# Optimization experiments

Hardware: AMD Instinct MI355X
Metric: run time of the kernel (lower is better)

Reference implementation:

```python
import jax, jax.numpy as jnp
import numpy as np

N_EMBD = 1024
N_HEAD = 16
HORIZON = 64
HS = N_EMBD // N_HEAD        # 64
BD = max(HS // 4, 16)        # 16


def setup_inputs() -> dict:
    key = jax.random.key(0)
    ks = jax.random.split(key, 12)
    s = 0.02
    B, T = 2, 1024
    return {
        "x": jax.random.normal(ks[0], (B, T, N_EMBD), jnp.float32),
        "W_disp": jax.random.normal(ks[1], (N_EMBD, N_HEAD * BD), jnp.float32) * s,
        "W_val": jax.random.normal(ks[2], (N_EMBD, N_EMBD), jnp.float32) * s,
        "rel_pos_emb": jax.random.normal(ks[3], (HORIZON, BD), jnp.float32) * s,
        "W_strain": jax.random.normal(ks[4], (BD, BD), jnp.float32) * s,
        "W_pos": jax.random.normal(ks[5], (BD, BD), jnp.float32) * s,
        "W_bond": jax.random.normal(ks[6], (BD, 1), jnp.float32) * s,
        "W_dmg": jax.random.normal(ks[7], (BD, BD), jnp.float32) * s,
        "b_dmg": jnp.zeros((BD,), jnp.float32),
        "W_dmg_out": jax.random.normal(ks[8], (BD, 1), jnp.float32) * s,
        "b_dmg_out": jnp.full((1,), -3.0, jnp.float32),  # nn.init.constant_(damage_out.bias, -3.0)
        "W_cproj": jax.random.normal(ks[9], (N_EMBD, N_EMBD), jnp.float32) * s,
    }


def _windows(t, delta):
    # t: (B, nh, T, D) -> (B, nh, T, delta, D); causal sliding window via left pad
    B, nh, T, D = t.shape
    padded = jnp.pad(t, ((0, 0), (0, 0), (delta - 1, 0), (0, 0)))
    idx = jnp.arange(T)[:, None] + jnp.arange(delta)[None, :]  # (T, delta)
    return padded[:, :, idx]  # gather over time axis


def reference(x, W_disp, W_val, rel_pos_emb, W_strain, W_pos, W_bond,
              W_dmg, b_dmg, W_dmg_out, b_dmg_out, W_cproj):
    B, T, C = x.shape
    nh, bd, hs = N_HEAD, BD, HS
    delta = min(HORIZON, T)

    disp = (x @ W_disp).reshape(B, T, nh, bd).transpose(0, 2, 1, 3)  # (B,nh,T,bd)
    val = (x @ W_val).reshape(B, T, nh, hs).transpose(0, 2, 1, 3)    # (B,nh,T,hs)

    disp_win = _windows(disp, delta)  # (B,nh,T,delta,bd)
    val_win = _windows(val, delta)    # (B,nh,T,delta,hs)

    # causal mask: window slot w for token t maps to position t - delta + 1 + w
    cmask = (jnp.arange(T)[:, None] - delta + 1 + jnp.arange(delta)[None, :]) >= 0  # (T,delta)

    strain = disp_win - disp[:, :, :, None, :]  # (B,nh,T,delta,bd)
    rel_emb = rel_pos_emb[:delta]               # (delta,bd)

    bond_act = jax.nn.gelu(strain @ W_strain + rel_emb @ W_pos, approximate=False)
    bond_logits = (bond_act @ W_bond)[..., 0]   # (B,nh,T,delta)

    damage_act = jax.nn.gelu(strain @ W_dmg + b_dmg, approximate=False)
    damage = jax.nn.sigmoid((damage_act @ W_dmg_out)[..., 0] + b_dmg_out[0])

    logits = bond_logits - 10.0 * damage
    logits = jnp.where(cmask[None, None], logits, -jnp.inf)
    weights = jax.nn.softmax(logits, axis=-1)

    out = jnp.einsum('bntd,bntde->bnte', weights, val_win)  # (B,nh,T,hs)
    out = out.transpose(0, 2, 1, 3).reshape(B, T, C)
    return out @ W_cproj
```

## Files before the change

kernel.cpp:

```cpp
#include <hip/hip_runtime.h>
#include <hip/hip_bf16.h>
#include <hip/hip_fp16.h>
#include <math.h>

#define TB   2
#define TT   1024
#define TC   1024
#define NH   16
#define HS   64
#define BDI  16
#define DLT  64
#define LDD  1280
#define GK   1024

typedef __attribute__((ext_vector_type(8))) short short8;
typedef __attribute__((ext_vector_type(4))) float floatx4;
typedef __attribute__((ext_vector_type(16))) float floatx16;
typedef __hip_bfloat16 bf16;

__device__ __forceinline__ unsigned pkbf(float a, float b) {
    return (__float_as_uint(a) >> 16) | (__float_as_uint(b) & 0xFFFF0000u);
}

__device__ __forceinline__ unsigned bfbits(float x) {
    bf16 h = __float2bfloat16(x);
    return (unsigned)*(unsigned short*)&h;
}

__device__ __forceinline__ __half2 gelu_pk(__half2 x, __half2 kc1, __half2 kc2,
                                           __half2 khalf) {
    __half2 y = __hmul2(x, x);
    __half2 p = __hfma2(y, kc2, kc1);
    return __hfma2(x, khalf, __hmul2(y, p));
}

__device__ __forceinline__ void gload_lds16(const void* g, void* l) {
    __builtin_amdgcn_global_load_lds(
        (const __attribute__((address_space(1))) unsigned int*)(unsigned long long)g,
        (__attribute__((address_space(3))) unsigned int*)(unsigned int)(unsigned long long)l,
        16, 0, 0);
}

__device__ __forceinline__ void tpose_body(const float* __restrict__ in,
                                           bf16* __restrict__ outp,
                                           int k0, int n0, int N,
                                           float (*tile)[33], int tid) {
    const int tx = tid & 31, ty4 = (tid >> 5) * 4;
#pragma unroll
    for (int i = 0; i < 4; i++)
        tile[ty4 + i][tx] = in[(long long)(k0 + ty4 + i) * N + n0 + tx];
    __syncthreads();
#pragma unroll
    for (int i = 0; i < 4; i++)
        outp[(long long)(n0 + ty4 + i) * TC + k0 + tx] = __float2bfloat16(tile[tx][ty4 + i]);
}

__global__ __launch_bounds__(256) void prep_k(
    const float* __restrict__ x, const float* __restrict__ Wdisp,
    const float* __restrict__ Wval, const float* __restrict__ Wc,
    bf16* __restrict__ xb, bf16* __restrict__ Wdvt, bf16* __restrict__ Wct) {
    __shared__ float tile[32][33];
    const int blk = blockIdx.x, tid = threadIdx.x;
    if (blk < 2048) {
        int i = blk * 1024 + tid * 4;
        float4 v = *(const float4*)(x + i);
        bf16 o0 = __float2bfloat16(v.x), o1 = __float2bfloat16(v.y);
        bf16 o2 = __float2bfloat16(v.z), o3 = __float2bfloat16(v.w);
        ushort4 u;
        u.x = *(unsigned short*)&o0; u.y = *(unsigned short*)&o1;
        u.z = *(unsigned short*)&o2; u.w = *(unsigned short*)&o3;
        *(ushort4*)(xb + i) = u;
    } else if (blk < 2304) {
        int l = blk - 2048;
        tpose_body(Wdisp, Wdvt, (l >> 3) * 32, (l & 7) * 32, 256, tile, tid);
    } else if (blk < 3328) {
        int l = blk - 2304;
        tpose_body(Wval, Wdvt + (size_t)256 * TC, (l >> 5) * 32, (l & 31) * 32, TC, tile, tid);
    } else {
        int l = blk - 3328;
        tpose_body(Wc, Wct, (l >> 5) * 32, (l & 31) * 32, TC, tile, tid);
    }
}

template <int ID>
__global__ __launch_bounds__(256) void mfma_gemm_k(const bf16* __restrict__ A,
                                                   const bf16* __restrict__ Bt,
                                                   float* __restrict__ C,
                                                   int M, int N, int nbx) {
    __shared__ __align__(16) bf16 As[2][64 * 128];
    __shared__ __align__(16) bf16 Bs[2][64 * 128];
    const int tid = threadIdx.x;
    const int w = tid >> 6, lane = tid & 63;

    const int xcd = blockIdx.x & 7, s0 = blockIdx.x >> 3;
    const int l = xcd * (gridDim.x >> 3) + s0;
    const int row0 = (l / nbx) * 64, col0 = (l % nbx) * 64;
    const int wm = (w >> 1) * 32, wn = (w & 1) * 32;

    const bf16* gA[4];
    const bf16* gB[4];
    int lofs[4];
#pragma unroll
    for (int p = 0; p < 4; p++) {
        int u = (p * 4 + w) * 64 + lane;
        int r = u >> 4, s = u & 15;
        int c = s ^ (r & 15);
        gA[p] = A  + (long long)(row0 + r) * GK + c * 8;
        gB[p] = Bt + (long long)(col0 + r) * GK + c * 8;
        lofs[p] = (p * 4 + w) * 512;
    }

    floatx4 acc[2][2] = {};
    const int rA = lane & 15, quad = lane >> 4;

#pragma unroll
    for (int p = 0; p < 4; p++) {
        gload_lds16(gA[p], &As[0][lofs[p]]);
        gload_lds16(gB[p], &Bs[0][lofs[p]]);
    }

    int cur = 0;
    for (int k0 = 0; k0 < GK; k0 += 128) {
        __syncthreads();
        if (k0 + 128 < GK) {
#pragma unroll
            for (int p = 0; p < 4; p++) {
                gload_lds16(gA[p] + k0 + 128, &As[cur ^ 1][lofs[p]]);
                gload_lds16(gB[p] + k0 + 128, &Bs[cur ^ 1][lofs[p]]);
            }
        }
        const bf16* Ac = As[cur];
        const bf16* Bc = Bs[cur];
#pragma unroll
        for (int kh = 0; kh < 4; kh++) {
            const int g = kh * 4 + quad;
            short8 af[2], bfr[2];
#pragma unroll
            for (int i = 0; i < 2; i++) {
                af[i]  = *(const short8*)&Ac[(wm + i * 16 + rA) * 128 + ((g ^ rA) * 8)];
                bfr[i] = *(const short8*)&Bc[(wn + i * 16 + rA) * 128 + ((g ^ rA) * 8)];
            }
#pragma unroll
            for (int i = 0; i < 2; i++)
#pragma unroll
                for (int j = 0; j < 2; j++)
                    acc[i][j] = __builtin_amdgcn_mfma_f32_16x16x32_bf16(af[i], bfr[j], acc[i][j], 0, 0, 0);
        }
        cur ^= 1;
    }
    const int cn = lane & 15, rq = (lane >> 4) * 4;
#pragma unroll
    for (int i = 0; i < 2; i++)
#pragma unroll
        for (int j = 0; j < 2; j++) {
            long long base = (long long)(row0 + wm + i * 16 + rq) * N + col0 + wn + j * 16 + cn;
#pragma unroll
            for (int r = 0; r < 4; r++)
                C[base + (long long)r * N] = acc[i][j][r];
        }
}

__global__ __launch_bounds__(256) void attn_k(
    const float* __restrict__ dv,
    const float* __restrict__ rel,
    const float* __restrict__ W_strain,
    const float* __restrict__ W_dmg,
    const float* __restrict__ Wp,
    const float* __restrict__ W_bond,
    const float* __restrict__ b_dmg,
    const float* __restrict__ W_dmg_out,
    const float* __restrict__ b_dmg_out,
    bf16* __restrict__ attnout) {
    __shared__ __align__(16) float          sDisp[79][20];
    __shared__ __align__(16) unsigned short sValT[64][104];
    __shared__ __align__(16) unsigned short sWgtS[16][104];

    const int tid = threadIdx.x;
    const int wave = tid >> 6, lane = tid & 63;
    const int xcd = blockIdx.x & 7, slot = blockIdx.x >> 3;
    const int bh = xcd * 4 + (slot >> 6);
    const int t0 = (slot & 63) * 16;
    const int h = bh & (NH - 1);
    const int b = bh >> 4;

    if (tid < 208) ((int4*)sWgtS)[tid] = make_int4(0, 0, 0, 0);

    for (int idx = tid; idx < 79 * 4; idx += 256) {
        int r = idx >> 2, c = idx & 3;
        int row = t0 - 63 + r; row = row < 0 ? 0 : row;
        *(float4*)&sDisp[r][c * 4] =
            *(const float4*)(dv + (long long)(b * TT + row) * LDD + h * BDI + c * 4);
    }
    for (int idx = tid; idx < 24 * 16; idx += 256) {
        int k4 = (idx >> 4) * 4, e4 = (idx & 15) * 4;
        float vv[4][4];
#pragma unroll
        for (int rr = 0; rr < 4; rr++) {
            int row = t0 - 63 + k4 + rr;
            row = row < 0 ? 0 : (row > TT - 1 ? TT - 1 : row);
            *(float4*)vv[rr] =
                *(const float4*)(dv + (long long)(b * TT + row) * LDD + 256 + h * HS + e4);
        }
#pragma unroll
        for (int e = 0; e < 4; e++) {
            uint2 wv;
            wv.x = bfbits(vv[0][e]) | (bfbits(vv[1][e]) << 16);
            wv.y = bfbits(vv[2][e]) | (bfbits(vv[3][e]) << 16);
            *(uint2*)&sValT[e4 + e][k4] = wv;
        }
    }

    const int n = lane & 31, hi = lane >> 5;
    union U8 { short8 s8; unsigned u[4]; };
    const floatx16 z16 = {};

    short8 aw, ape;
    {
        const float* wsel = (n < 16) ? (W_strain + n) : (W_dmg + (n - 16));
        float wv[8], pv[8];
#pragma unroll
        for (int e = 0; e < 8; e++) {
            wv[e] = wsel[(8 * hi + e) * BDI];
            pv[e] = (n < 16) ? Wp[(8 * hi + e) * BDI + n] : 0.f;
        }
        U8 a, p;
#pragma unroll
        for (int q = 0; q < 4; q++) {
            a.u[q] = pkbf(wv[2 * q], wv[2 * q + 1]);
            p.u[q] = pkbf(pv[2 * q], pv[2 * q + 1]);
        }
        aw = a.s8; ape = p.s8;
    }
    floatx16 cb[2];
#pragma unroll
    for (int h2 = 0; h2 < 2; h2++) {
        float rv[8];
        const float* rp = rel + (32 * h2 + n) * BDI + 8 * hi;
        *(float4*)&rv[0] = *(const float4*)rp;
        *(float4*)&rv[4] = *(const float4*)(rp + 4);
        U8 r_;
#pragma unroll
        for (int q = 0; q < 4; q++) r_.u[q] = pkbf(rv[2 * q], rv[2 * q + 1]);
        cb[h2] = __builtin_amdgcn_mfma_f32_32x32x16_bf16(ape, r_.s8, z16, 0, 0, 0);
    }
    {
        float4 bdA = *(const float4*)(b_dmg + 4 * hi);
        float4 bdB = *(const float4*)(b_dmg + 8 + 4 * hi);
#pragma unroll
        for (int h2 = 0; h2 < 2; h2++) {
            cb[h2][8]  += bdA.x; cb[h2][9]  += bdA.y;
            cb[h2][10] += bdA.z; cb[h2][11] += bdA.w;
            cb[h2][12] += bdB.x; cb[h2][13] += bdB.y;
            cb[h2][14] += bdB.z; cb[h2][15] += bdB.w;
        }
    }
    __half2 wbp[4], wdp[4];
    {
        float4 wbA = *(const float4*)(W_bond + 4 * hi);
        float4 wbB = *(const float4*)(W_bond + 8 + 4 * hi);
        float4 wdA = *(const float4*)(W_dmg_out + 4 * hi);
        float4 wdB = *(const float4*)(W_dmg_out + 8 + 4 * hi);
        wbp[0] = __floats2half2_rn(wbA.x, wbA.y); wbp[1] = __floats2half2_rn(wbA.z, wbA.w);
        wbp[2] = __floats2half2_rn(wbB.x, wbB.y); wbp[3] = __floats2half2_rn(wbB.z, wbB.w);
        wdp[0] = __floats2half2_rn(wdA.x, wdA.y); wdp[1] = __floats2half2_rn(wdA.z, wdA.w);
        wdp[2] = __floats2half2_rn(wdB.x, wdB.y); wdp[3] = __floats2half2_rn(wdB.z, wdB.w);
    }
    const float bdo0 = b_dmg_out[0];
    const __half2 kc1   = __floats2half2_rn(0.3989422804f, 0.3989422804f);
    const __half2 kc2   = __floats2half2_rn(-0.06649038006f, -0.06649038006f);
    const __half2 khalf = __floats2half2_rn(0.5f, 0.5f);

    __syncthreads();

#pragma unroll
    for (int s = 0; s < 4; s++) {
        const int tau = 4 * wave + s;
        float oc[8];
        {
            const float* op = &sDisp[tau + 63][8 * hi];
            *(float4*)&oc[0] = *(const float4*)op;
            *(float4*)&oc[4] = *(const float4*)(op + 4);
        }
        floatx16 c2r[2];
#pragma unroll
        for (int h2 = 0; h2 < 2; h2++) {
            const float* rp = &sDisp[tau + 32 * h2 + n][8 * hi];
            float p[8];
            *(float4*)&p[0] = *(const float4*)rp;
            *(float4*)&p[4] = *(const float4*)(rp + 4);
            U8 t_;
#pragma unroll
            for (int pp = 0; pp < 4; pp++)
                t_.u[pp] = pkbf(p[2 * pp] - oc[2 * pp], p[2 * pp + 1] - oc[2 * pp + 1]);
            c2r[h2] = __builtin_amdgcn_mfma_f32_32x32x16_bf16(aw, t_.s8, cb[h2], 0, 0, 0);
        }
        float ee[2];
#pragma unroll
        for (int h2 = 0; h2 < 2; h2++) {
            __half2 accb = __floats2half2_rn(0.f, 0.f);
            __half2 accd = __floats2half2_rn(0.f, 0.f);
#pragma unroll
            for (int i = 0; i < 4; i++) {
                __half2 xb_ = __floats2half2_rn(c2r[h2][2 * i], c2r[h2][2 * i + 1]);
                __half2 xd_ = __floats2half2_rn(c2r[h2][8 + 2 * i], c2r[h2][9 + 2 * i]);
                accb = __hfma2(gelu_pk(xb_, kc1, kc2, khalf), wbp[i], accb);
                accd = __hfma2(gelu_pk(xd_, kc1, kc2, khalf), wdp[i], accd);
            }
            float bond = __low2float(accb) + __high2float(accb);
            float dmgv = __low2float(accd) + __high2float(accd);
            bond += __shfl_xor(bond, 32);
            dmgv += __shfl_xor(dmgv, 32);
            float damage = 1.f / (1.f + __expf(-(dmgv + bdo0)));
            const int j = 32 * h2 + n;
            const bool valid = (t0 + tau + j - 63) >= 0;
            ee[h2] = valid ? __expf(bond - 10.f * damage) : 0.f;
        }
        float sm = ee[0] + ee[1];
#pragma unroll
        for (int off = 16; off >= 1; off >>= 1) sm += __shfl_xor(sm, off);
        float inv = 1.0f / sm;
        if (hi == 0) {
            sWgtS[tau][tau + n]      = (unsigned short)bfbits(ee[0] * inv);
            sWgtS[tau][tau + 32 + n] = (unsigned short)bfbits(ee[1] * inv);
        }
    }
    __syncthreads();

    const int m = lane & 15, quad = lane >> 4;
    const floatx4 zf = {0.f, 0.f, 0.f, 0.f};
    floatx4 acc = zf;
#pragma unroll
    for (int c = 0; c < 3; c++) {
        short8 afr = *(const short8*)&sWgtS[m][c * 32 + quad * 8];
        short8 bfr = *(const short8*)&sValT[16 * wave + m][c * 32 + quad * 8];
        acc = __builtin_amdgcn_mfma_f32_16x16x32_bf16(afr, bfr, acc, 0, 0, 0);
    }
    const int e0 = 16 * wave + m;
#pragma unroll
    for (int r = 0; r < 4; r++) {
        int tau = quad * 4 + r;
        attnout[(long long)(b * TT + t0 + tau) * TC + h * HS + e0] = __float2bfloat16(acc[r]);
    }
}

extern "C" void kernel_launch(void* const* d_in, const int* in_sizes, int n_in,
                              void* d_out, int out_size, void* d_ws, size_t ws_size,
                              hipStream_t stream) {
    const float* x      = (const float*)d_in[0];
    const float* W_disp = (const float*)d_in[1];
    const float* W_val  = (const float*)d_in[2];
    const float* rel    = (const float*)d_in[3];
    const float* Ws     = (const float*)d_in[4];
    const float* Wp     = (const float*)d_in[5];
    const float* Wb     = (const float*)d_in[6];
    const float* Wd     = (const float*)d_in[7];
    const float* bd_    = (const float*)d_in[8];
    const float* Wdo    = (const float*)d_in[9];
    const float* bdo    = (const float*)d_in[10];
    const float* Wc     = (const float*)d_in[11];
    float* out = (float*)d_out;

    const int M = TB * TT;
    char* ws = (char*)d_ws;
    bf16*  xb    = (bf16*)ws;
    bf16*  attnb = (bf16*)ws;
    bf16*  Wdvt  = (bf16*)(ws + (size_t)4 * 1024 * 1024);
    bf16*  Wct   = (bf16*)(ws + (size_t)6656 * 1024);
    float* dvC   = (float*)(ws + (size_t)8704 * 1024);

    dim3 blk(256);
    prep_k<<<4352, blk, 0, stream>>>(x, W_disp, W_val, Wc, xb, Wdvt, Wct);
    mfma_gemm_k<1><<<(M / 64) * (LDD / 64), blk, 0, stream>>>(xb, Wdvt, dvC, M, LDD, LDD / 64);
    attn_k<<<(TB * NH * TT) / 16, blk, 0, stream>>>(dvC, rel, Ws, Wd, Wp, Wb, bd_,
                                                    Wdo, bdo, attnb);
    mfma_gemm_k<2><<<(M / 64) * (TC / 64), blk, 0, stream>>>(attnb, Wct, out, M, TC, TC / 64);
}
```

Before: 135.8 us.

## Emit transposed bf16 values from QKV GEMM epilogue and precompute positional bias

The first GEMM now writes the value projection directly as per-head transposed bf16 (head, e, t). The attention kernel can then read MFMA B fragments straight from global memory instead of staging and converting them through shared memory. The rel_pos_emb @ W_pos product is precomputed once in the prep kernel and added in fp16 rather than computed per block with an MFMA. The change also adds an occupancy hint (launch_bounds 256,8) and shifts the weight-column indexing by one slot. In exchange it adds uncoalesced short global writes in the GEMM epilogue and unstaged global reads of values in attention.

Measured after the change: 131.8 us. 2.9% less time.

```diff
diff --git a/kernel.cpp b/kernel.cpp
--- a/kernel.cpp
+++ b/kernel.cpp
@@ -10,8 +10,8 @@
 #define HS   64
 #define BDI  16
 #define DLT  64
-#define LDD  1280
 #define GK   1024
+#define NDV  1280
 
 typedef __attribute__((ext_vector_type(8))) short short8;
 typedef __attribute__((ext_vector_type(4))) float floatx4;
@@ -58,7 +58,9 @@
 __global__ __launch_bounds__(256) void prep_k(
     const float* __restrict__ x, const float* __restrict__ Wdisp,
     const float* __restrict__ Wval, const float* __restrict__ Wc,
-    bf16* __restrict__ xb, bf16* __restrict__ Wdvt, bf16* __restrict__ Wct) {
+    const float* __restrict__ rel, const float* __restrict__ Wp,
+    bf16* __restrict__ xb, bf16* __restrict__ Wdvt, bf16* __restrict__ Wct,
+    float* __restrict__ peG) {
     __shared__ float tile[32][33];
     const int blk = blockIdx.x, tid = threadIdx.x;
     if (blk < 2048) {
@@ -76,9 +78,17 @@
     } else if (blk < 3328) {
         int l = blk - 2304;
         tpose_body(Wval, Wdvt + (size_t)256 * TC, (l >> 5) * 32, (l & 31) * 32, TC, tile, tid);
-    } else {
+    } else if (blk < 4352) {
         int l = blk - 3328;
         tpose_body(Wc, Wct, (l >> 5) * 32, (l & 31) * 32, TC, tile, tid);
+    } else {
+        int idx = (blk - 4352) * 256 + tid;
+        int j = idx >> 4, d = idx & 15;
+        float s = 0.f;
+#pragma unroll
+        for (int k = 0; k < BDI; k++)
+            s += rel[j * BDI + k] * Wp[k * BDI + d];
+        peG[idx] = s;
     }
 }
 
@@ -86,6 +96,7 @@
 __global__ __launch_bounds__(256) void mfma_gemm_k(const bf16* __restrict__ A,
                                                    const bf16* __restrict__ Bt,
                                                    float* __restrict__ C,
+                                                   bf16* __restrict__ valT,
                                                    int M, int N, int nbx) {
     __shared__ __align__(16) bf16 As[2][64 * 128];
     __shared__ __align__(16) bf16 Bs[2][64 * 128];
@@ -149,30 +160,45 @@
         cur ^= 1;
     }
     const int cn = lane & 15, rq = (lane >> 4) * 4;
-#pragma unroll
-    for (int i = 0; i < 2; i++)
-#pragma unroll
-        for (int j = 0; j < 2; j++) {
-            long long base = (long long)(row0 + wm + i * 16 + rq) * N + col0 + wn + j * 16 + cn;
-#pragma unroll
-            for (int r = 0; r < 4; r++)
-                C[base + (long long)r * N] = acc[i][j][r];
-        }
-}
-
-__global__ __launch_bounds__(256) void attn_k(
-    const float* __restrict__ dv,
-    const float* __restrict__ rel,
+    if (ID == 1 && col0 >= 256) {
+        const int hh = (col0 - 256) >> 6;
+        const int bb = row0 >> 10;
+#pragma unroll
+        for (int i = 0; i < 2; i++)
+#pragma unroll
+            for (int j = 0; j < 2; j++) {
+                int e = wn + j * 16 + cn;
+                int trow = row0 - bb * TT + wm + i * 16 + rq;
+                uint2 st;
+                st.x = bfbits(acc[i][j][0]) | (bfbits(acc[i][j][1]) << 16);
+                st.y = bfbits(acc[i][j][2]) | (bfbits(acc[i][j][3]) << 16);
+                *(uint2*)(valT + ((size_t)((bb * NH + hh) * HS + e) * TT + trow)) = st;
+            }
+    } else {
+#pragma unroll
+        for (int i = 0; i < 2; i++)
+#pragma unroll
+            for (int j = 0; j < 2; j++) {
+                long long base = (long long)(row0 + wm + i * 16 + rq) * N + col0 + wn + j * 16 + cn;
+#pragma unroll
+                for (int r = 0; r < 4; r++)
+                    C[base + (long long)r * N] = acc[i][j][r];
+            }
+    }
+}
+
+__global__ __launch_bounds__(256, 8) void attn_k(
+    const float* __restrict__ dispC,
+    const bf16* __restrict__ valT,
+    const float* __restrict__ peG,
     const float* __restrict__ W_strain,
     const float* __restrict__ W_dmg,
-    const float* __restrict__ Wp,
     const float* __restrict__ W_bond,
     const float* __restrict__ b_dmg,
     const float* __restrict__ W_dmg_out,
     const float* __restrict__ b_dmg_out,
     bf16* __restrict__ attnout) {
     __shared__ __align__(16) float          sDisp[79][20];
-    __shared__ __align__(16) unsigned short sValT[64][104];
     __shared__ __align__(16) unsigned short sWgtS[16][104];
 
     const int tid = threadIdx.x;
@@ -189,73 +215,38 @@
         int r = idx >> 2, c = idx & 3;
         int row = t0 - 63 + r; row = row < 0 ? 0 : row;
         *(float4*)&sDisp[r][c * 4] =
-            *(const float4*)(dv + (long long)(b * TT + row) * LDD + h * BDI + c * 4);
-    }
-    for (int idx = tid; idx < 24 * 16; idx += 256) {
-        int k4 = (idx >> 4) * 4, e4 = (idx & 15) * 4;
-        float vv[4][4];
-#pragma unroll
-        for (int rr = 0; rr < 4; rr++) {
-            int row = t0 - 63 + k4 + rr;
-            row = row < 0 ? 0 : (row > TT - 1 ? TT - 1 : row);
-            *(float4*)vv[rr] =
-                *(const float4*)(dv + (long long)(b * TT + row) * LDD + 256 + h * HS + e4);
-        }
-#pragma unroll
-        for (int e = 0; e < 4; e++) {
-            uint2 wv;
-            wv.x = bfbits(vv[0][e]) | (bfbits(vv[1][e]) << 16);
-            wv.y = bfbits(vv[2][e]) | (bfbits(vv[3][e]) << 16);
-            *(uint2*)&sValT[e4 + e][k4] = wv;
-        }
+            *(const float4*)(dispC + (long long)(b * TT + row) * 256 + h * BDI + c * 4);
     }
 
     const int n = lane & 31, hi = lane >> 5;
     union U8 { short8 s8; unsigned u[4]; };
     const floatx16 z16 = {};
 
-    short8 aw, ape;
+    short8 aw;
     {
         const float* wsel = (n < 16) ? (W_strain + n) : (W_dmg + (n - 16));
-        float wv[8], pv[8];
-#pragma unroll
-        for (int e = 0; e < 8; e++) {
-            wv[e] = wsel[(8 * hi + e) * BDI];
-            pv[e] = (n < 16) ? Wp[(8 * hi + e) * BDI + n] : 0.f;
-        }
-        U8 a, p;
-#pragma unroll
-        for (int q = 0; q < 4; q++) {
-            a.u[q] = pkbf(wv[2 * q], wv[2 * q + 1]);
-            p.u[q] = pkbf(pv[2 * q], pv[2 * q + 1]);
-        }
-        aw = a.s8; ape = p.s8;
-    }
-    floatx16 cb[2];
+        float wv[8];
+#pragma unroll
+        for (int e = 0; e < 8; e++) wv[e] = wsel[(8 * hi + e) * BDI];
+        U8 a;
+#pragma unroll
+        for (int q = 0; q < 4; q++) a.u[q] = pkbf(wv[2 * q], wv[2 * q + 1]);
+        aw = a.s8;
+    }
+    __half2 pbb[2][4], pbd[4], wbp[4], wdp[4];
 #pragma unroll
     for (int h2 = 0; h2 < 2; h2++) {
-        float rv[8];
-        const float* rp = rel + (32 * h2 + n) * BDI + 8 * hi;
-        *(float4*)&rv[0] = *(const float4*)rp;
-        *(float4*)&rv[4] = *(const float4*)(rp + 4);
-        U8 r_;
-#pragma unroll
-        for (int q = 0; q < 4; q++) r_.u[q] = pkbf(rv[2 * q], rv[2 * q + 1]);
-        cb[h2] = __builtin_amdgcn_mfma_f32_32x32x16_bf16(ape, r_.s8, z16, 0, 0, 0);
+        const float* pj = peG + (n + 32 * h2) * BDI;
+        float4 A_ = *(const float4*)(pj + 4 * hi);
+        float4 B_ = *(const float4*)(pj + 8 + 4 * hi);
+        pbb[h2][0] = __floats2half2_rn(A_.x, A_.y); pbb[h2][1] = __floats2half2_rn(A_.z, A_.w);
+        pbb[h2][2] = __floats2half2_rn(B_.x, B_.y); pbb[h2][3] = __floats2half2_rn(B_.z, B_.w);
     }
     {
         float4 bdA = *(const float4*)(b_dmg + 4 * hi);
         float4 bdB = *(const float4*)(b_dmg + 8 + 4 * hi);
-#pragma unroll
-        for (int h2 = 0; h2 < 2; h2++) {
-            cb[h2][8]  += bdA.x; cb[h2][9]  += bdA.y;
-            cb[h2][10] += bdA.z; cb[h2][11] += bdA.w;
-            cb[h2][12] += bdB.x; cb[h2][13] += bdB.y;
-            cb[h2][14] += bdB.z; cb[h2][15] += bdB.w;
-        }
-    }
-    __half2 wbp[4], wdp[4];
-    {
+        pbd[0] = __floats2half2_rn(bdA.x, bdA.y); pbd[1] = __floats2half2_rn(bdA.z, bdA.w);
+        pbd[2] = __floats2half2_rn(bdB.x, bdB.y); pbd[3] = __floats2half2_rn(bdB.z, bdB.w);
         float4 wbA = *(const float4*)(W_bond + 4 * hi);
         float4 wbB = *(const float4*)(W_bond + 8 + 4 * hi);
         float4 wdA = *(const float4*)(W_dmg_out + 4 * hi);
@@ -281,7 +272,7 @@
             *(float4*)&oc[0] = *(const float4*)op;
             *(float4*)&oc[4] = *(const float4*)(op + 4);
         }
-        floatx16 c2r[2];
+        float ee[2];
 #pragma unroll
         for (int h2 = 0; h2 < 2; h2++) {
             const float* rp = &sDisp[tau + 32 * h2 + n][8 * hi];
@@ -292,17 +283,13 @@
 #pragma unroll
             for (int pp = 0; pp < 4; pp++)
                 t_.u[pp] = pkbf(p[2 * pp] - oc[2 * pp], p[2 * pp + 1] - oc[2 * pp + 1]);
-            c2r[h2] = __builtin_amdgcn_mfma_f32_32x32x16_bf16(aw, t_.s8, cb[h2], 0, 0, 0);
-        }
-        float ee[2];
-#pragma unroll
-        for (int h2 = 0; h2 < 2; h2++) {
+            floatx16 c2 = __builtin_amdgcn_mfma_f32_32x32x16_bf16(aw, t_.s8, z16, 0, 0, 0);
             __half2 accb = __floats2half2_rn(0.f, 0.f);
             __half2 accd = __floats2half2_rn(0.f, 0.f);
 #pragma unroll
             for (int i = 0; i < 4; i++) {
-                __half2 xb_ = __floats2half2_rn(c2r[h2][2 * i], c2r[h2][2 * i + 1]);
-                __half2 xd_ = __floats2half2_rn(c2r[h2][8 + 2 * i], c2r[h2][9 + 2 * i]);
+                __half2 xb_ = __hadd2(__floats2half2_rn(c2[2 * i], c2[2 * i + 1]), pbb[h2][i]);
+                __half2 xd_ = __hadd2(__floats2half2_rn(c2[8 + 2 * i], c2[9 + 2 * i]), pbd[i]);
                 accb = __hfma2(gelu_pk(xb_, kc1, kc2, khalf), wbp[i], accb);
                 accd = __hfma2(gelu_pk(xd_, kc1, kc2, khalf), wdp[i], accd);
             }
@@ -320,19 +307,22 @@
         for (int off = 16; off >= 1; off >>= 1) sm += __shfl_xor(sm, off);
         float inv = 1.0f / sm;
         if (hi == 0) {
-            sWgtS[tau][tau + n]      = (unsigned short)bfbits(ee[0] * inv);
-            sWgtS[tau][tau + 32 + n] = (unsigned short)bfbits(ee[1] * inv);
+            sWgtS[tau][tau + 1 + n]  = (unsigned short)bfbits(ee[0] * inv);
+            sWgtS[tau][tau + 33 + n] = (unsigned short)bfbits(ee[1] * inv);
         }
     }
     __syncthreads();
 
     const int m = lane & 15, quad = lane >> 4;
     const floatx4 zf = {0.f, 0.f, 0.f, 0.f};
+    const bf16* vbase = valT + ((size_t)(b * NH + h) * HS + 16 * wave + m) * TT;
     floatx4 acc = zf;
 #pragma unroll
     for (int c = 0; c < 3; c++) {
+        int toff = t0 - 64 + c * 32 + quad * 8;
+        toff = toff < 0 ? 0 : (toff > TT - 8 ? TT - 8 : toff);
         short8 afr = *(const short8*)&sWgtS[m][c * 32 + quad * 8];
-        short8 bfr = *(const short8*)&sValT[16 * wave + m][c * 32 + quad * 8];
+        short8 bfr = *(const short8*)(vbase + toff);
         acc = __builtin_amdgcn_mfma_f32_16x16x32_bf16(afr, bfr, acc, 0, 0, 0);
     }
     const int e0 = 16 * wave + m;
@@ -366,12 +356,15 @@
     bf16*  attnb = (bf16*)ws;
     bf16*  Wdvt  = (bf16*)(ws + (size_t)4 * 1024 * 1024);
     bf16*  Wct   = (bf16*)(ws + (size_t)6656 * 1024);
-    float* dvC   = (float*)(ws + (size_t)8704 * 1024);
+    float* dispC = (float*)(ws + (size_t)8704 * 1024);
+    bf16*  valT  = (bf16*)(ws + (size_t)10752 * 1024);
+    float* peG   = (float*)(ws + (size_t)14848 * 1024);
 
     dim3 blk(256);
-    prep_k<<<4352, blk, 0, stream>>>(x, W_disp, W_val, Wc, xb, Wdvt, Wct);
-    mfma_gemm_k<1><<<(M / 64) * (LDD / 64), blk, 0, stream>>>(xb, Wdvt, dvC, M, LDD, LDD / 64);
-    attn_k<<<(TB * NH * TT) / 16, blk, 0, stream>>>(dvC, rel, Ws, Wd, Wp, Wb, bd_,
+    prep_k<<<4356, blk, 0, stream>>>(x, W_disp, W_val, Wc, rel, Wp,
+                                     xb, Wdvt, Wct, peG);
+    mfma_gemm_k<1><<<(M / 64) * (NDV / 64), blk, 0, stream>>>(xb, Wdvt, dispC, valT, M, 256, NDV / 64);
+    attn_k<<<(TB * NH * TT) / 16, blk, 0, stream>>>(dispC, valT, peG, Ws, Wd, Wb, bd_,
                                                     Wdo, bdo, attnb);
-    mfma_gemm_k<2><<<(M / 64) * (TC / 64), blk, 0, stream>>>(attnb, Wct, out, M, TC, TC / 64);
-}
+    mfma_gemm_k<2><<<(M / 64) * (TC / 64), blk, 0, stream>>>(attnb, Wct, out, nullptr, M, TC, TC / 64);
+}
```
